# Kernel tuning notes

Measured on AMD Instinct MI355X. Metric: run time of the kernel, lower is better.

The kernel has to match this reference:

```python
import jax, jax.numpy as jnp
import numpy as np

N_NODES = 10000
N_EDGES = 200000
NODE_DIM = 128
EDGE_DIM = 16
CONV_DIM = 64
HEADS = 5
NEG_SLOPE = 0.2


def gatv2_layer(x, src, dst, edge_attr, Wl, bl, We, att, bias):
    # PyG GATv2Conv, share_weights=True, concat=False, add_self_loops=True, eval mode
    N = x.shape[0]
    H, C = att.shape
    xl = (x @ Wl + bl).reshape(N, H, C)  # [N,H,C]; x_r = x_l (share_weights)
    # self loops, edge_attr fill_value='mean' (mean of incoming edge_attr per node)
    deg = jax.ops.segment_sum(jnp.ones(dst.shape[0], x.dtype), dst, num_segments=N)
    loop_attr = jax.ops.segment_sum(edge_attr, dst, num_segments=N) / jnp.maximum(deg, 1.0)[:, None]
    loop = jnp.arange(N, dtype=src.dtype)
    src_f = jnp.concatenate([src, loop])
    dst_f = jnp.concatenate([dst, loop])
    ea = jnp.concatenate([edge_attr, loop_attr], axis=0)
    e_emb = (ea @ We).reshape(-1, H, C)  # [E+N,H,C]
    m = jax.nn.leaky_relu(xl[src_f] + xl[dst_f] + e_emb, NEG_SLOPE)
    score = jnp.einsum('ehc,hc->eh', m, att)  # [E+N,H]
    # per-destination softmax over incoming edges
    smax = jax.ops.segment_max(score, dst_f, num_segments=N)
    ex = jnp.exp(score - smax[dst_f])
    denom = jax.ops.segment_sum(ex, dst_f, num_segments=N)
    alpha = ex / denom[dst_f]
    out = jax.ops.segment_sum(alpha[:, :, None] * xl[src_f], dst_f, num_segments=N)
    return out.mean(axis=1) + bias  # concat=False -> mean over heads


def setup_inputs() -> dict:
    key = jax.random.key(0)
    ks = jax.random.split(key, 32)
    inp = {
        'x': jax.random.normal(ks[0], (N_NODES, NODE_DIM), jnp.float32),
        'edge_index': jax.random.randint(ks[1], (2, N_EDGES), 0, N_NODES, dtype=jnp.int32),
        'edge_attr': jax.random.normal(ks[2], (N_EDGES, EDGE_DIM), jnp.float32),
    }
    in_dims = [NODE_DIM, CONV_DIM, CONV_DIM]
    HC = HEADS * CONV_DIM
    k = 3
    for l in range(3):
        d = in_dims[l]
        inp[f'Wl{l}'] = jax.random.normal(ks[k], (d, HC), jnp.float32) / np.float32(np.sqrt(d)); k += 1
        inp[f'bl{l}'] = jnp.zeros((HC,), jnp.float32)
        inp[f'We{l}'] = jax.random.normal(ks[k], (EDGE_DIM, HC), jnp.float32) / np.float32(np.sqrt(EDGE_DIM)); k += 1
        inp[f'att{l}'] = jax.random.normal(ks[k], (HEADS, CONV_DIM), jnp.float32) / np.float32(np.sqrt(CONV_DIM)); k += 1
        inp[f'b{l}'] = jnp.zeros((CONV_DIM,), jnp.float32)
    return inp


def reference(x, edge_index, edge_attr,
              Wl0, bl0, We0, att0, b0,
              Wl1, bl1, We1, att1, b1,
              Wl2, bl2, We2, att2, b2):
    src, dst = edge_index[0], edge_index[1]
    h = x
    layers = [(Wl0, bl0, We0, att0, b0), (Wl1, bl1, We1, att1, b1), (Wl2, bl2, We2, att2, b2)]
    for Wl, bl, We, att, b in layers:
        h = gatv2_layer(h, src, dst, edge_attr, Wl, bl, We, att, b)
        h = jax.nn.elu(h)
    return h
```

## Files before the change

kernel.cpp:

```cpp
#include <hip/hip_runtime.h>
#include <hip/hip_bf16.h>


#define NN 10000
#define NE 200000
#define ND 128
#define ED 16
#define CD 64
#define NH 5
#define HC 320
#define EF 210000
#define EFP 210048
#define NEG 0.2f
#define SB 103

__global__ void k_count(const int* __restrict__ dst, int* __restrict__ deg) {
  int e = blockIdx.x * blockDim.x + threadIdx.x;
  if (e >= NE) return;
  atomicAdd(&deg[dst[e]], 1);
}

__global__ __launch_bounds__(1024) void k_scan(const int* __restrict__ deg,
                                               int* __restrict__ rowptr) {
  __shared__ int part[1024];
  int t = threadIdx.x;
  int base = t * 10;
  int local[10];
  int s = 0;
  #pragma unroll
  for (int j = 0; j < 10; j++) {
    int i = base + j;
    local[j] = (i < NN) ? deg[i] : 0;
    s += local[j];
  }
  part[t] = s;
  __syncthreads();
  for (int off = 1; off < 1024; off <<= 1) {
    int v = (t >= off) ? part[t - off] : 0;
    __syncthreads();
    part[t] += v;
    __syncthreads();
  }
  int prefix = (t > 0) ? part[t - 1] : 0;
  #pragma unroll
  for (int j = 0; j < 10; j++) {
    int i = base + j;
    if (i < NN) rowptr[i] = prefix;
    prefix += local[j];
  }
  if (t == 1023) rowptr[NN] = prefix;
}

__global__ void k_fill(const int* __restrict__ ei, const int* __restrict__ rowptr,
                       int* __restrict__ cursor, int* __restrict__ csr_eid,
                       int* __restrict__ csr_src, int* __restrict__ csr_dst) {
  int e = blockIdx.x * blockDim.x + threadIdx.x;
  if (e >= NE) return;
  int d = ei[NE + e];
  int slot = atomicAdd(&cursor[d], 1);
  int pos = rowptr[d] + slot;
  csr_eid[pos] = e;
  csr_src[pos] = ei[e];
  csr_dst[pos] = d;
}

__global__ __launch_bounds__(256) void k_loopattr(const int* __restrict__ csr_eid,
                                                  const int* __restrict__ rowptr,
                                                  const float* __restrict__ eattr,
                                                  float* __restrict__ loop_attr) {
  int wave = threadIdx.x >> 6, lane = threadIdx.x & 63;
  int d = blockIdx.x * 4 + wave;
  if (d >= NN) return;
  int g = lane >> 4, k = lane & 15;
  int b = rowptr[d], n = rowptr[d + 1] - b;
  float s = 0.f;
  for (int i = g; i < n; i += 4)
    s += eattr[(size_t)csr_eid[b + i] * ED + k];
  s += __shfl_xor(s, 16, 64);
  s += __shfl_xor(s, 32, 64);
  if (g == 0) loop_attr[d * ED + k] = s / fmaxf((float)n, 1.0f);
}

__global__ void k_eacsr(const int* __restrict__ csr_eid, const float* __restrict__ eattr,
                        float* __restrict__ ea_csr) {
  int idx = blockIdx.x * blockDim.x + threadIdx.x;
  if (idx >= NE * 4) return;
  int p = idx >> 2, q = idx & 3;
  const float4* sp = (const float4*)(eattr + (size_t)csr_eid[p] * ED);
  ((float4*)(ea_csr + (size_t)p * ED))[q] = sp[q];
}

__global__ void k_wet(const float* __restrict__ We, float* __restrict__ WeT) {
  int i = blockIdx.x * blockDim.x + threadIdx.x;
  if (i >= ED * HC) return;
  int hc = i >> 4, k = i & 15;
  WeT[i] = We[k * HC + hc];
}

template <int D>
__global__ __launch_bounds__(320) void k_xl(const float* __restrict__ h,
                                            const float* __restrict__ Wl,
                                            const float* __restrict__ bl,
                                            float* __restrict__ xl) {
  constexpr int NPB = 8;
  int node0 = blockIdx.x * NPB;
  int t = threadIdx.x;
  float acc[NPB];
  #pragma unroll
  for (int i = 0; i < NPB; i++) acc[i] = 0.f;
  for (int k = 0; k < D; k += 4) {
    float w0 = Wl[(k + 0) * HC + t];
    float w1 = Wl[(k + 1) * HC + t];
    float w2 = Wl[(k + 2) * HC + t];
    float w3 = Wl[(k + 3) * HC + t];
    #pragma unroll
    for (int i = 0; i < NPB; i++) {
      float4 hv = *(const float4*)(h + (size_t)(node0 + i) * D + k);
      acc[i] += hv.x * w0 + hv.y * w1 + hv.z * w2 + hv.w * w3;
    }
  }
  float bv = bl[t];
  #pragma unroll
  for (int i = 0; i < NPB; i++)
    xl[(size_t)(node0 + i) * HC + t] = acc[i] + bv;
}

__device__ __forceinline__ float dot4(float4 a, float4 b) {
  return a.x * b.x + a.y * b.y + a.z * b.z + a.w * b.w;
}

__global__ __launch_bounds__(256) void k_score(
    const int* __restrict__ csr_src, const int* __restrict__ csr_dst,
    const float* __restrict__ ea_csr, const float* __restrict__ loop_attr,
    const float* __restrict__ xl, const float* __restrict__ WeT,
    const float* __restrict__ att, float* __restrict__ wP) {
  int bid = blockIdx.x;
  int lb = (bid & 7) * SB + (bid >> 3);
  int p = lb * 256 + threadIdx.x;
  if (p >= EF) return;
  int h = blockIdx.y;
  int s, d;
  const float* ea;
  if (p < NE) { s = csr_src[p]; d = csr_dst[p]; ea = ea_csr + (size_t)p * ED; }
  else        { s = d = p - NE; ea = loop_attr + (size_t)(p - NE) * ED; }
  float4 ea4[4];
  {
    const float4* q = (const float4*)ea;
    ea4[0] = q[0]; ea4[1] = q[1]; ea4[2] = q[2]; ea4[3] = q[3];
  }
  const float* xsrow = xl + (size_t)s * HC + h * CD;
  const float* xdrow = xl + (size_t)d * HC + h * CD;
  const float* wrow  = WeT + h * CD * ED;
  const float* arow  = att + h * CD;
  float sc = 0.f;
  #pragma unroll 4
  for (int cb = 0; cb < CD; cb += 4) {
    float4 xs4 = *(const float4*)(xsrow + cb);
    float4 xd4 = *(const float4*)(xdrow + cb);
    const float4* w0 = (const float4*)(wrow + (cb + 0) * ED);
    const float4* w1 = (const float4*)(wrow + (cb + 1) * ED);
    const float4* w2 = (const float4*)(wrow + (cb + 2) * ED);
    const float4* w3 = (const float4*)(wrow + (cb + 3) * ED);
    float z0 = xs4.x + xd4.x + dot4(ea4[0], w0[0]) + dot4(ea4[1], w0[1]) +
               dot4(ea4[2], w0[2]) + dot4(ea4[3], w0[3]);
    float z1 = xs4.y + xd4.y + dot4(ea4[0], w1[0]) + dot4(ea4[1], w1[1]) +
               dot4(ea4[2], w1[2]) + dot4(ea4[3], w1[3]);
    float z2 = xs4.z + xd4.z + dot4(ea4[0], w2[0]) + dot4(ea4[1], w2[1]) +
               dot4(ea4[2], w2[2]) + dot4(ea4[3], w2[3]);
    float z3 = xs4.w + xd4.w + dot4(ea4[0], w3[0]) + dot4(ea4[1], w3[1]) +
               dot4(ea4[2], w3[2]) + dot4(ea4[3], w3[3]);
    z0 *= (z0 > 0.f) ? 1.0f : NEG;
    z1 *= (z1 > 0.f) ? 1.0f : NEG;
    z2 *= (z2 > 0.f) ? 1.0f : NEG;
    z3 *= (z3 > 0.f) ? 1.0f : NEG;
    float4 a4 = *(const float4*)(arow + cb);
    sc += a4.x * z0 + a4.y * z1 + a4.z * z2 + a4.w * z3;
  }
  sc = fminf(fmaxf(sc, -60.f), 60.f);
  wP[(size_t)h * EFP + p] = __expf(sc);
}

__global__ __launch_bounds__(320) void k_agg(
    const int* __restrict__ csr_src, const int* __restrict__ rowptr,
    const float* __restrict__ wP, const float* __restrict__ xl,
    const float* __restrict__ bias, float* __restrict__ out) {
  __shared__ float s_v[NH][CD];
  int h = threadIdx.x >> 6, lane = threadIdx.x & 63;
  int d = blockIdx.x;
  int b = rowptr[d], n = rowptr[d + 1] - b;
  const float* sp = wP + (size_t)h * EFP;
  const float* xlh = xl + h * CD + lane;
  float dn = sp[NE + d];
  float acc = dn * xlh[(size_t)d * HC];
  int p = b, pe = b + n;
  for (; p + 4 <= pe; p += 4) {
    int s0 = csr_src[p], s1 = csr_src[p + 1], s2 = csr_src[p + 2], s3 = csr_src[p + 3];
    float w0 = sp[p], w1 = sp[p + 1], w2 = sp[p + 2], w3 = sp[p + 3];
    float x0 = xlh[(size_t)s0 * HC];
    float x1 = xlh[(size_t)s1 * HC];
    float x2 = xlh[(size_t)s2 * HC];
    float x3 = xlh[(size_t)s3 * HC];
    dn += (w0 + w1) + (w2 + w3);
    acc += w0 * x0 + w1 * x1 + w2 * x2 + w3 * x3;
  }
  for (; p < pe; p++) {
    int s0 = csr_src[p];
    float w0 = sp[p];
    dn += w0;
    acc += w0 * xlh[(size_t)s0 * HC];
  }
  s_v[h][lane] = acc / dn;
  __syncthreads();
  if (h == 0) {
    float v = s_v[0][lane] + s_v[1][lane] + s_v[2][lane] + s_v[3][lane] + s_v[4][lane];
    v = v * (1.0f / NH) + bias[lane];
    v = v > 0.f ? v : expm1f(v);
    out[(size_t)d * CD + lane] = v;
  }
}

extern "C" void kernel_launch(void* const* d_in, const int* in_sizes, int n_in,
                              void* d_out, int out_size, void* d_ws, size_t ws_size,
                              hipStream_t stream) {
  const float* x = (const float*)d_in[0];
  const int* ei = (const int*)d_in[1];
  const float* eattr = (const float*)d_in[2];

  char* w = (char*)d_ws;
  int* degi      = (int*)w;                 w += NN * 4;
  int* cursor    = (int*)w;                 w += NN * 4;
  int* rowptr    = (int*)w;                 w += (NN + 1) * 4;
  int* csr_eid   = (int*)w;                 w += NE * 4;
  int* csr_src   = (int*)w;                 w += NE * 4;
  int* csr_dst   = (int*)w;                 w += NE * 4;
  float* loop_attr = (float*)w;             w += (size_t)NN * ED * 4;
  float* ea_csr  = (float*)w;               w += (size_t)NE * ED * 4;
  float* xl      = (float*)w;               w += (size_t)NN * HC * 4;
  float* wPbuf   = (float*)w;               w += (size_t)NH * EFP * 4;
  float* WeT     = (float*)w;               w += (size_t)ED * HC * 4;
  float* hbuf    = (float*)w;               w += (size_t)NN * CD * 4;

  hipMemsetAsync(degi, 0, NN * 4, stream);
  hipMemsetAsync(cursor, 0, NN * 4, stream);
  k_count<<<(NE + 255) / 256, 256, 0, stream>>>(ei + NE, degi);
  k_scan<<<1, 1024, 0, stream>>>(degi, rowptr);
  k_fill<<<(NE + 255) / 256, 256, 0, stream>>>(ei, rowptr, cursor, csr_eid, csr_src, csr_dst);
  k_loopattr<<<(NN + 3) / 4, 256, 0, stream>>>(csr_eid, rowptr, eattr, loop_attr);
  k_eacsr<<<(NE * 4 + 255) / 256, 256, 0, stream>>>(csr_eid, eattr, ea_csr);

  for (int l = 0; l < 3; l++) {
    const float* Wl  = (const float*)d_in[3 + 5 * l];
    const float* bl  = (const float*)d_in[4 + 5 * l];
    const float* We  = (const float*)d_in[5 + 5 * l];
    const float* att = (const float*)d_in[6 + 5 * l];
    const float* b   = (const float*)d_in[7 + 5 * l];

    k_wet<<<(ED * HC + 255) / 256, 256, 0, stream>>>(We, WeT);
    if (l == 0) k_xl<ND><<<NN / 8, 320, 0, stream>>>(x, Wl, bl, xl);
    else        k_xl<CD><<<NN / 8, 320, 0, stream>>>(hbuf, Wl, bl, xl);

    dim3 gs(8 * SB, NH);
    k_score<<<gs, 256, 0, stream>>>(csr_src, csr_dst, ea_csr, loop_attr,
                                    xl, WeT, att, wPbuf);

    float* dst_out = (l < 2) ? hbuf : (float*)d_out;
    k_agg<<<NN, 320, 0, stream>>>(csr_src, rowptr, wPbuf, xl, b, dst_out);
  }
}
```

Before: 528.7 us.

## Fuse next-layer linear projection into aggregation and batch weight transposes

The aggregation kernel now also applies the next layer's Wl projection per node from a shared-memory copy of the ELU output, writing xl for the following layer into a ping-pong buffer. This removes two separate k_xl launches and the round trip through hbuf. The three We transposes are merged into one launch at the start. The trade-off is that each aggregation block does a 64x320 matvec per node and rereads Wl from cache.

```diff
diff --git a/kernel.cpp b/kernel.cpp
--- a/kernel.cpp
+++ b/kernel.cpp
@@ -90,11 +90,14 @@
   ((float4*)(ea_csr + (size_t)p * ED))[q] = sp[q];
 }
 
-__global__ void k_wet(const float* __restrict__ We, float* __restrict__ WeT) {
+__global__ void k_wet3(const float* __restrict__ We0, const float* __restrict__ We1,
+                       const float* __restrict__ We2, float* __restrict__ WeT) {
   int i = blockIdx.x * blockDim.x + threadIdx.x;
-  if (i >= ED * HC) return;
-  int hc = i >> 4, k = i & 15;
-  WeT[i] = We[k * HC + hc];
+  if (i >= 3 * ED * HC) return;
+  int l = i / (ED * HC), r = i % (ED * HC);
+  int hc = r >> 4, k = r & 15;
+  const float* src = (l == 0) ? We0 : (l == 1) ? We1 : We2;
+  WeT[i] = src[k * HC + hc];
 }
 
 template <int D>
@@ -180,19 +183,24 @@
   wP[(size_t)h * EFP + p] = __expf(sc);
 }
 
-__global__ __launch_bounds__(320) void k_agg(
+template <bool LAST>
+__global__ __launch_bounds__(320) void k_aggxl(
     const int* __restrict__ csr_src, const int* __restrict__ rowptr,
-    const float* __restrict__ wP, const float* __restrict__ xl,
-    const float* __restrict__ bias, float* __restrict__ out) {
+    const float* __restrict__ wP, const float* __restrict__ xl_in,
+    const float* __restrict__ bias,
+    const float* __restrict__ Wl, const float* __restrict__ bl,
+    float* __restrict__ outp) {
   __shared__ float s_v[NH][CD];
-  int h = threadIdx.x >> 6, lane = threadIdx.x & 63;
+  __shared__ float s_h[CD];
+  int t = threadIdx.x;
+  int h = t >> 6, lane = t & 63;
   int d = blockIdx.x;
-  int b = rowptr[d], n = rowptr[d + 1] - b;
+  int b0 = rowptr[d], n = rowptr[d + 1] - b0;
   const float* sp = wP + (size_t)h * EFP;
-  const float* xlh = xl + h * CD + lane;
+  const float* xlh = xl_in + h * CD + lane;
   float dn = sp[NE + d];
   float acc = dn * xlh[(size_t)d * HC];
-  int p = b, pe = b + n;
+  int p = b0, pe = b0 + n;
   for (; p + 4 <= pe; p += 4) {
     int s0 = csr_src[p], s1 = csr_src[p + 1], s2 = csr_src[p + 2], s3 = csr_src[p + 3];
     float w0 = sp[p], w1 = sp[p + 1], w2 = sp[p + 2], w3 = sp[p + 3];
@@ -211,11 +219,20 @@
   }
   s_v[h][lane] = acc / dn;
   __syncthreads();
-  if (h == 0) {
-    float v = s_v[0][lane] + s_v[1][lane] + s_v[2][lane] + s_v[3][lane] + s_v[4][lane];
-    v = v * (1.0f / NH) + bias[lane];
+  if (t < CD) {
+    float v = s_v[0][t] + s_v[1][t] + s_v[2][t] + s_v[3][t] + s_v[4][t];
+    v = v * (1.0f / NH) + bias[t];
     v = v > 0.f ? v : expm1f(v);
-    out[(size_t)d * CD + lane] = v;
+    if constexpr (LAST) outp[(size_t)d * CD + t] = v;
+    else s_h[t] = v;
+  }
+  if constexpr (!LAST) {
+    __syncthreads();
+    float a2 = bl[t];
+    #pragma unroll 8
+    for (int k = 0; k < CD; k++)
+      a2 += s_h[k] * Wl[k * HC + t];
+    outp[(size_t)d * HC + t] = a2;
   }
 }
 
@@ -235,10 +252,23 @@
   int* csr_dst   = (int*)w;                 w += NE * 4;
   float* loop_attr = (float*)w;             w += (size_t)NN * ED * 4;
   float* ea_csr  = (float*)w;               w += (size_t)NE * ED * 4;
-  float* xl      = (float*)w;               w += (size_t)NN * HC * 4;
+  float* xlA     = (float*)w;               w += (size_t)NN * HC * 4;
+  float* xlB     = (float*)w;               w += (size_t)NN * HC * 4;
   float* wPbuf   = (float*)w;               w += (size_t)NH * EFP * 4;
-  float* WeT     = (float*)w;               w += (size_t)ED * HC * 4;
-  float* hbuf    = (float*)w;               w += (size_t)NN * CD * 4;
+  float* WeT     = (float*)w;               w += (size_t)3 * ED * HC * 4;
+
+  const float* Wl0  = (const float*)d_in[3];
+  const float* bl0  = (const float*)d_in[4];
+  const float* att0 = (const float*)d_in[6];
+  const float* b0   = (const float*)d_in[7];
+  const float* Wl1  = (const float*)d_in[8];
+  const float* bl1  = (const float*)d_in[9];
+  const float* att1 = (const float*)d_in[11];
+  const float* b1   = (const float*)d_in[12];
+  const float* Wl2  = (const float*)d_in[13];
+  const float* bl2  = (const float*)d_in[14];
+  const float* att2 = (const float*)d_in[16];
+  const float* b2   = (const float*)d_in[17];
 
   hipMemsetAsync(degi, 0, NN * 4, stream);
   hipMemsetAsync(cursor, 0, NN * 4, stream);
@@ -247,23 +277,22 @@
   k_fill<<<(NE + 255) / 256, 256, 0, stream>>>(ei, rowptr, cursor, csr_eid, csr_src, csr_dst);
   k_loopattr<<<(NN + 3) / 4, 256, 0, stream>>>(csr_eid, rowptr, eattr, loop_attr);
   k_eacsr<<<(NE * 4 + 255) / 256, 256, 0, stream>>>(csr_eid, eattr, ea_csr);
-
-  for (int l = 0; l < 3; l++) {
-    const float* Wl  = (const float*)d_in[3 + 5 * l];
-    const float* bl  = (const float*)d_in[4 + 5 * l];
-    const float* We  = (const float*)d_in[5 + 5 * l];
-    const float* att = (const float*)d_in[6 + 5 * l];
-    const float* b   = (const float*)d_in[7 + 5 * l];
-
-    k_wet<<<(ED * HC + 255) / 256, 256, 0, stream>>>(We, WeT);
-    if (l == 0) k_xl<ND><<<NN / 8, 320, 0, stream>>>(x, Wl, bl, xl);
-    else        k_xl<CD><<<NN / 8, 320, 0, stream>>>(hbuf, Wl, bl, xl);
-
-    dim3 gs(8 * SB, NH);
-    k_score<<<gs, 256, 0, stream>>>(csr_src, csr_dst, ea_csr, loop_attr,
-                                    xl, WeT, att, wPbuf);
-
-    float* dst_out = (l < 2) ? hbuf : (float*)d_out;
-    k_agg<<<NN, 320, 0, stream>>>(csr_src, rowptr, wPbuf, xl, b, dst_out);
-  }
-}
+  k_wet3<<<(3 * ED * HC + 255) / 256, 256, 0, stream>>>(
+      (const float*)d_in[5], (const float*)d_in[10], (const float*)d_in[15], WeT);
+
+  k_xl<ND><<<NN / 8, 320, 0, stream>>>(x, Wl0, bl0, xlA);
+
+  dim3 gs(8 * SB, NH);
+  k_score<<<gs, 256, 0, stream>>>(csr_src, csr_dst, ea_csr, loop_attr,
+                                  xlA, WeT, att0, wPbuf);
+  k_aggxl<false><<<NN, 320, 0, stream>>>(csr_src, rowptr, wPbuf, xlA, b0,
+                                         Wl1, bl1, xlB);
+  k_score<<<gs, 256, 0, stream>>>(csr_src, csr_dst, ea_csr, loop_attr,
+                                  xlB, WeT + ED * HC, att1, wPbuf);
+  k_aggxl<false><<<NN, 320, 0, stream>>>(csr_src, rowptr, wPbuf, xlB, b1,
+                                         Wl2, bl2, xlA);
+  k_score<<<gs, 256, 0, stream>>>(csr_src, csr_dst, ea_csr, loop_attr,
+                                  xlA, WeT + 2 * ED * HC, att2, wPbuf);
+  k_aggxl<true><<<NN, 320, 0, stream>>>(csr_src, rowptr, wPbuf, xlA, b2,
+                                        nullptr, nullptr, (float*)d_out);
+}
```

Result: no change. 533.9 us (+1.0%).
